# Performance work log

Hardware: AMD Instinct MI355X
Metric: run time of the kernel (lower is better)

Reference implementation:

```python
import jax, jax.numpy as jnp
import numpy as np

H = 1024   # hidden_size
B = 4096   # batch
C = 2      # num_classes

def setup_inputs() -> dict:
    key = jax.random.key(0)
    ks = jax.random.split(key, 12)
    s = 0.02
    return {
        "h": jax.random.normal(ks[0], (2, B, H), jnp.float32),
        "c": jax.random.normal(ks[1], (2, B, H), jnp.float32),
        # torch nn.LSTM params: W_ih_l0 (4H, C), W_hh_l0 (4H, H), biases (4H,)
        "W_ih0": jax.random.normal(ks[2], (4 * H, C), jnp.float32) * s,
        "W_hh0": jax.random.normal(ks[3], (4 * H, H), jnp.float32) * s,
        "b_ih0": jax.random.normal(ks[4], (4 * H,), jnp.float32) * s,
        "b_hh0": jax.random.normal(ks[5], (4 * H,), jnp.float32) * s,
        "W_ih1": jax.random.normal(ks[6], (4 * H, H), jnp.float32) * s,
        "W_hh1": jax.random.normal(ks[7], (4 * H, H), jnp.float32) * s,
        "b_ih1": jax.random.normal(ks[8], (4 * H,), jnp.float32) * s,
        "b_hh1": jax.random.normal(ks[9], (4 * H,), jnp.float32) * s,
        "fc_W": jax.random.normal(ks[10], (C, H), jnp.float32) * s,
        "fc_b": jax.random.normal(ks[11], (C,), jnp.float32) * s,
        "pred_len": 64,
    }

def _lstm_cell(gates, c_prev):
    # torch gate order: input, forget, cell(g), output
    i, f, g, o = jnp.split(gates, 4, axis=1)
    c_new = jax.nn.sigmoid(f) * c_prev + jax.nn.sigmoid(i) * jnp.tanh(g)
    h_new = jax.nn.sigmoid(o) * jnp.tanh(c_new)
    return h_new, c_new

def reference(h, c, W_ih0, W_hh0, b_ih0, b_hh0, W_ih1, W_hh1, b_ih1, b_hh1, fc_W, fc_b, pred_len):
    h0, h1 = h[0], h[1]
    c0, c1 = c[0], c[1]
    x0 = jnp.zeros((h0.shape[0], fc_W.shape[0]), h.dtype)  # (B, C)

    def step(carry, _):
        h0, c0, h1, c1, x = carry
        g0 = x @ W_ih0.T + b_ih0 + h0 @ W_hh0.T + b_hh0
        h0n, c0n = _lstm_cell(g0, c0)
        g1 = h0n @ W_ih1.T + b_ih1 + h1 @ W_hh1.T + b_hh1
        h1n, c1n = _lstm_cell(g1, c1)
        logit = h1n @ fc_W.T + fc_b                       # (B, C)
        # greedy argmax feedback (targets=None branch)
        x_next = jax.nn.one_hot(jnp.argmax(logit, axis=1), logit.shape[1], dtype=logit.dtype)
        return (h0n, c0n, h1n, c1n, x_next), logit

    _, logits = jax.lax.scan(step, (h0, c0, h1, c1, x0), None, length=pred_len)
    return jnp.transpose(logits, (1, 0, 2))  # (B, pred_len, C)
```

## Files before the change

### kernel.cpp

```cpp
#include <hip/hip_runtime.h>
#include <stdint.h>

#define H_ 1024
#define NG_ 4096

typedef float f32x4 __attribute__((ext_vector_type(4)));
typedef __bf16 bf16x8 __attribute__((ext_vector_type(8)));

__device__ __forceinline__ unsigned short f2bf(float f) {
  union { float f; uint32_t u; } v; v.f = f;
  uint32_t r = v.u + 0x7FFFu + ((v.u >> 16) & 1u);
  return (unsigned short)(r >> 16);
}
__device__ __forceinline__ float bf2f(unsigned short b) {
  union { uint32_t u; float f; } v; v.u = ((uint32_t)b) << 16; return v.f;
}

__device__ __forceinline__ void gload_lds16(const void* g, void* l) {
  __builtin_amdgcn_global_load_lds(
      (const __attribute__((address_space(1))) void*)g,
      (__attribute__((address_space(3))) void*)l, 16, 0, 0);
}

__device__ __forceinline__ float sigm(float x) { return 1.f / (1.f + __expf(-x)); }
__device__ __forceinline__ float tanh_(float x) { return 1.f - 2.f / (__expf(2.f * x) + 1.f); }

__global__ void prep_w0(const float* __restrict__ Whh0, unsigned short* __restrict__ Wr) {
  int i = (blockIdx.x * 256 + threadIdx.x) * 4;
  int r = i >> 10, k = i & 1023;
  int gate = (r >> 4) & 3;
  int j = ((r >> 6) << 4) + (r & 15);
  const float4 v = *(const float4*)(Whh0 + (size_t)(gate * H_ + j) * H_ + k);
  ushort4 o; o.x = f2bf(v.x); o.y = f2bf(v.y); o.z = f2bf(v.z); o.w = f2bf(v.w);
  *(ushort4*)(Wr + i) = o;
}

__global__ void prep_wcat(const float* __restrict__ Wih1, const float* __restrict__ Whh1,
                          unsigned short* __restrict__ Wr) {
  int i = (blockIdx.x * 256 + threadIdx.x) * 4;
  int r = i >> 11, k = i & 2047;
  int gate = (r >> 4) & 3;
  int j = ((r >> 6) << 4) + (r & 15);
  const float* src = (k < 1024) ? (Wih1 + (size_t)(gate * H_ + j) * H_ + k)
                                : (Whh1 + (size_t)(gate * H_ + j) * H_ + (k - 1024));
  const float4 v = *(const float4*)src;
  ushort4 o; o.x = f2bf(v.x); o.y = f2bf(v.y); o.z = f2bf(v.z); o.w = f2bf(v.w);
  *(ushort4*)(Wr + (size_t)r * 2048 + k) = o;
}

__global__ void prep_small(const float* __restrict__ Wih0,
                           const float* __restrict__ bih0, const float* __restrict__ bhh0,
                           const float* __restrict__ bih1, const float* __restrict__ bhh1,
                           float* __restrict__ bias0r, float* __restrict__ bias1r,
                           float* __restrict__ wi0r) {
  int r = blockIdx.x * 256 + threadIdx.x;
  int gate = (r >> 4) & 3;
  int j = ((r >> 6) << 4) + (r & 15);
  int old = gate * H_ + j;
  bias0r[r] = bih0[old] + bhh0[old];
  bias1r[r] = bih1[old] + bhh1[old];
  wi0r[r * 2 + 0] = Wih0[old * 2 + 0];
  wi0r[r * 2 + 1] = Wih0[old * 2 + 1];
}

__global__ void prep_state(const float* __restrict__ h, const float* __restrict__ c,
                           unsigned short* __restrict__ h0b, unsigned short* __restrict__ h1b,
                           float* __restrict__ c0, float* __restrict__ c1, int bh) {
  int i = (blockIdx.x * 256 + threadIdx.x) * 4;
  float4 a = *(const float4*)(h + i);
  float4 b = *(const float4*)(h + (size_t)bh + i);
  ushort4 oa; oa.x = f2bf(a.x); oa.y = f2bf(a.y); oa.z = f2bf(a.z); oa.w = f2bf(a.w);
  ushort4 ob; ob.x = f2bf(b.x); ob.y = f2bf(b.y); ob.z = f2bf(b.z); ob.w = f2bf(b.w);
  *(ushort4*)(h0b + i) = oa;
  *(ushort4*)(h1b + i) = ob;
  *(float4*)(c0 + i) = *(const float4*)(c + i);
  *(float4*)(c1 + i) = *(const float4*)(c + (size_t)bh + i);
}

__global__ void lstm_gemm_cell(const unsigned short* __restrict__ A0,
                               const unsigned short* __restrict__ A1,
                               int Ktot,
                               const unsigned short* __restrict__ Bw,
                               const float* __restrict__ biasr,
                               const float* __restrict__ wi0r,
                               const int* __restrict__ xidx,
                               int have_x,
                               float* __restrict__ Cst,
                               unsigned short* __restrict__ Hout) {
  __shared__ unsigned short As[128 * 64];
  __shared__ unsigned short Bs[128 * 64];
  const int tid  = threadIdx.x;
  const int lane = tid & 63;
  const int wv   = tid >> 6;
  const int wm   = wv >> 1, wn = wv & 1;
  const int tile_m = blockIdx.y * 128;
  const int tile_n = blockIdx.x * 128;

  f32x4 acc[4][4];
#pragma unroll
  for (int m = 0; m < 4; ++m)
#pragma unroll
    for (int n = 0; n < 4; ++n) acc[m][n] = (f32x4)0.f;

  const int lrow = lane >> 3;
  const int lk   = (lane & 7) * 8;

  const int nk = Ktot >> 6;
  for (int kt = 0; kt < nk; ++kt) {
    const int k0 = kt << 6;
    const unsigned short* Ap; int kl;
    if (k0 < 1024) { Ap = A0; kl = k0; } else { Ap = A1; kl = k0 - 1024; }
#pragma unroll
    for (int i = 0; i < 4; ++i) {
      int chunk = wv * 4 + i;
      int row = chunk * 8 + lrow;
      gload_lds16(Ap + (size_t)(tile_m + row) * H_ + kl + lk, (void*)&As[chunk * 512]);
    }
#pragma unroll
    for (int i = 0; i < 4; ++i) {
      int chunk = wv * 4 + i;
      int row = chunk * 8 + lrow;
      gload_lds16(Bw + (size_t)(tile_n + row) * Ktot + k0 + lk, (void*)&Bs[chunk * 512]);
    }
    __syncthreads();

    const char* Ab = (const char*)As;
    const char* Bb = (const char*)Bs;
    const int arow = wm * 64 + (lane & 15);
    const int brow = wn * 64 + (lane & 15);
    const int koff = (lane >> 4) * 16;
#pragma unroll
    for (int ks = 0; ks < 2; ++ks) {
      bf16x8 af[4], bfr[4];
#pragma unroll
      for (int m = 0; m < 4; ++m)
        af[m] = *(const bf16x8*)(Ab + (arow + m * 16) * 128 + ks * 64 + koff);
#pragma unroll
      for (int n = 0; n < 4; ++n)
        bfr[n] = *(const bf16x8*)(Bb + (brow + n * 16) * 128 + ks * 64 + koff);
#pragma unroll
      for (int m = 0; m < 4; ++m)
#pragma unroll
        for (int n = 0; n < 4; ++n)
          acc[m][n] = __builtin_amdgcn_mfma_f32_16x16x32_bf16(af[m], bfr[n], acc[m][n], 0, 0, 0);
    }
    __syncthreads();
  }

  const int cl = lane & 15;
  const int rq = (lane >> 4) * 4;
  const int jgrp = (tile_n >> 6) + wn;
  const int j = jgrp * 16 + cl;
  float bias[4], w0v[4] = {0,0,0,0}, w1v[4] = {0,0,0,0};
#pragma unroll
  for (int n = 0; n < 4; ++n) {
    int colr = tile_n + wn * 64 + n * 16 + cl;
    bias[n] = biasr[colr];
    if (have_x) { w0v[n] = wi0r[colr * 2]; w1v[n] = wi0r[colr * 2 + 1]; }
  }
#pragma unroll
  for (int m = 0; m < 4; ++m) {
#pragma unroll
    for (int q = 0; q < 4; ++q) {
      int row = tile_m + wm * 64 + m * 16 + rq + q;
      float gi = acc[m][0][q] + bias[0];
      float gf = acc[m][1][q] + bias[1];
      float gg = acc[m][2][q] + bias[2];
      float go = acc[m][3][q] + bias[3];
      if (have_x) {
        int x = xidx[row];
        gi += x ? w1v[0] : w0v[0];
        gf += x ? w1v[1] : w0v[1];
        gg += x ? w1v[2] : w0v[2];
        go += x ? w1v[3] : w0v[3];
      }
      size_t off = (size_t)row * H_ + j;
      float cp = Cst[off];
      float cn = sigm(gf) * cp + sigm(gi) * tanh_(gg);
      float hn = sigm(go) * tanh_(cn);
      Cst[off] = cn;
      Hout[off] = f2bf(hn);
    }
  }
}

__global__ void fc_argmax(const unsigned short* __restrict__ h1,
                          const float* __restrict__ fcW, const float* __restrict__ fcb,
                          float* __restrict__ out, int* __restrict__ xidx,
                          int t, int pred_len) {
  const int lane = threadIdx.x & 63;
  const int wv = threadIdx.x >> 6;
  const int row = blockIdx.x * 4 + wv;
  const unsigned short* hp = h1 + (size_t)row * H_ + lane * 16;
  float d0 = 0.f, d1 = 0.f;
#pragma unroll
  for (int u = 0; u < 2; ++u) {
    ushort4 ha = *(const ushort4*)(hp + u * 8);
    ushort4 hb = *(const ushort4*)(hp + u * 8 + 4);
    float hv[8] = { bf2f(ha.x), bf2f(ha.y), bf2f(ha.z), bf2f(ha.w),
                    bf2f(hb.x), bf2f(hb.y), bf2f(hb.z), bf2f(hb.w) };
#pragma unroll
    for (int e = 0; e < 8; ++e) {
      int k = lane * 16 + u * 8 + e;
      d0 += hv[e] * fcW[k];
      d1 += hv[e] * fcW[H_ + k];
    }
  }
#pragma unroll
  for (int off = 32; off > 0; off >>= 1) {
    d0 += __shfl_xor(d0, off);
    d1 += __shfl_xor(d1, off);
  }
  if (lane == 0) {
    d0 += fcb[0]; d1 += fcb[1];
    size_t o = ((size_t)row * pred_len + t) * 2;
    out[o] = d0; out[o + 1] = d1;
    xidx[row] = (d1 > d0) ? 1 : 0;
  }
}

extern "C" void kernel_launch(void* const* d_in, const int* in_sizes, int n_in,
                              void* d_out, int out_size, void* d_ws, size_t ws_size,
                              hipStream_t stream) {
  const float* h     = (const float*)d_in[0];
  const float* c     = (const float*)d_in[1];
  const float* Wih0  = (const float*)d_in[2];
  const float* Whh0  = (const float*)d_in[3];
  const float* bih0  = (const float*)d_in[4];
  const float* bhh0  = (const float*)d_in[5];
  const float* Wih1  = (const float*)d_in[6];
  const float* Whh1  = (const float*)d_in[7];
  const float* bih1  = (const float*)d_in[8];
  const float* bhh1  = (const float*)d_in[9];
  const float* fcW   = (const float*)d_in[10];
  const float* fcb   = (const float*)d_in[11];

  const int B = in_sizes[0] / (2 * H_);
  const int pred_len = out_size / (B * 2);
  const int BH = B * H_;

  size_t off = 0;
  auto carve = [&](size_t bytes) -> void* {
    void* p = (char*)d_ws + off;
    off += (bytes + 255) & ~(size_t)255;
    return p;
  };
  unsigned short* Whh0r = (unsigned short*)carve((size_t)NG_ * 1024 * 2);
  unsigned short* Wcatr = (unsigned short*)carve((size_t)NG_ * 2048 * 2);
  unsigned short* h0b[2], *h1b[2];
  h0b[0] = (unsigned short*)carve((size_t)BH * 2);
  h0b[1] = (unsigned short*)carve((size_t)BH * 2);
  h1b[0] = (unsigned short*)carve((size_t)BH * 2);
  h1b[1] = (unsigned short*)carve((size_t)BH * 2);
  float* c0 = (float*)carve((size_t)BH * 4);
  float* c1 = (float*)carve((size_t)BH * 4);
  float* bias0r = (float*)carve(NG_ * 4);
  float* bias1r = (float*)carve(NG_ * 4);
  float* wi0r   = (float*)carve(NG_ * 2 * 4);
  int*   xidx   = (int*)carve(B * 4);

  hipLaunchKernelGGL(prep_w0,   dim3((NG_ * 1024 / 4) / 256), dim3(256), 0, stream, Whh0, Whh0r);
  hipLaunchKernelGGL(prep_wcat, dim3((NG_ * 2048 / 4) / 256), dim3(256), 0, stream, Wih1, Whh1, Wcatr);
  hipLaunchKernelGGL(prep_small, dim3(NG_ / 256), dim3(256), 0, stream,
                     Wih0, bih0, bhh0, bih1, bhh1, bias0r, bias1r, wi0r);
  hipLaunchKernelGGL(prep_state, dim3((BH / 4) / 256), dim3(256), 0, stream,
                     h, c, h0b[0], h1b[0], c0, c1, BH);

  dim3 ggrid(NG_ / 128, B / 128);
  dim3 gblk(256);
  float* out = (float*)d_out;

  for (int t = 0; t < pred_len; ++t) {
    const int cur = t & 1, nxt = cur ^ 1;
    hipLaunchKernelGGL(lstm_gemm_cell, ggrid, gblk, 0, stream,
                       h0b[cur], (const unsigned short*)nullptr, 1024, Whh0r,
                       bias0r, wi0r, xidx, (t > 0) ? 1 : 0, c0, h0b[nxt]);
    hipLaunchKernelGGL(lstm_gemm_cell, ggrid, gblk, 0, stream,
                       h0b[nxt], h1b[cur], 2048, Wcatr,
                       bias1r, (const float*)nullptr, (const int*)nullptr, 0, c1, h1b[nxt]);
    hipLaunchKernelGGL(fc_argmax, dim3(B / 4), dim3(256), 0, stream,
                       h1b[nxt], fcW, fcb, out, xidx, t, pred_len);
  }
}
```

Measured before the change: 8.484 ms.

## Use 256x256 tiles with double-buffered swizzled LDS and async prefetch

The fused LSTM GEMM+cell kernel moves from 128x128 tiles with 4 waves to 256x256 tiles with 8 waves. Global-to-LDS loads are double-buffered two K-steps ahead using explicit waitcnt and barriers, and the LDS layout gets an XOR swizzle to avoid bank conflicts. The aim is to hide load latency behind MFMA and raise data reuse per byte. The cost is 128 KB of LDS and 256 grid blocks per launch, which lowers occupancy and may leave many CUs idle.

```diff
diff --git a/kernel.cpp b/kernel.cpp
--- a/kernel.cpp
+++ b/kernel.cpp
@@ -77,81 +77,116 @@
   *(float4*)(c1 + i) = *(const float4*)(c + (size_t)bh + i);
 }
 
-__global__ void lstm_gemm_cell(const unsigned short* __restrict__ A0,
-                               const unsigned short* __restrict__ A1,
-                               int Ktot,
-                               const unsigned short* __restrict__ Bw,
-                               const float* __restrict__ biasr,
-                               const float* __restrict__ wi0r,
-                               const int* __restrict__ xidx,
-                               int have_x,
-                               float* __restrict__ Cst,
-                               unsigned short* __restrict__ Hout) {
-  __shared__ unsigned short As[128 * 64];
-  __shared__ unsigned short Bs[128 * 64];
+__global__ void __launch_bounds__(512, 2)
+lstm_gemm_cell(const unsigned short* __restrict__ A0,
+               const unsigned short* __restrict__ A1,
+               int Ktot,
+               const unsigned short* __restrict__ Bw,
+               const float* __restrict__ biasr,
+               const float* __restrict__ wi0r,
+               const int* __restrict__ xidx,
+               int have_x,
+               float* __restrict__ Cst,
+               unsigned short* __restrict__ Hout) {
+  __shared__ unsigned short As[2][256 * 64];
+  __shared__ unsigned short Bs[2][256 * 64];
+
   const int tid  = threadIdx.x;
   const int lane = tid & 63;
   const int wv   = tid >> 6;
-  const int wm   = wv >> 1, wn = wv & 1;
-  const int tile_m = blockIdx.y * 128;
-  const int tile_n = blockIdx.x * 128;
-
-  f32x4 acc[4][4];
-#pragma unroll
-  for (int m = 0; m < 4; ++m)
+  const int wm   = wv >> 2;
+  const int wn   = wv & 3;
+  const int tile_m = blockIdx.y * 256;
+  const int tile_n = blockIdx.x * 256;
+
+  const int rowt = tid >> 3;
+  const int cb8  = (tid & 7) * 8;
+  const int ce   = (((tid & 7) ^ (rowt & 7)) * 8);
+
+  const int NK = Ktot >> 6;
+
+  auto stage = [&](int d, int kt) {
+    const int kb = kt << 6;
+    const unsigned short* Ap = A0; int kl = kb;
+    if (kb >= 1024) { Ap = A1; kl = kb - 1024; }
+#pragma unroll
+    for (int i = 0; i < 4; ++i) {
+      const int row = i * 64 + rowt;
+      gload_lds16(Ap + (size_t)(tile_m + row) * H_ + kl + ce, (void*)&As[d][row * 64 + cb8]);
+    }
+#pragma unroll
+    for (int i = 0; i < 4; ++i) {
+      const int row = i * 64 + rowt;
+      gload_lds16(Bw + (size_t)(tile_n + row) * (size_t)Ktot + kb + ce, (void*)&Bs[d][row * 64 + cb8]);
+    }
+  };
+
+  f32x4 acc[8][4];
+#pragma unroll
+  for (int m = 0; m < 8; ++m)
 #pragma unroll
     for (int n = 0; n < 4; ++n) acc[m][n] = (f32x4)0.f;
 
-  const int lrow = lane >> 3;
-  const int lk   = (lane & 7) * 8;
-
-  const int nk = Ktot >> 6;
-  for (int kt = 0; kt < nk; ++kt) {
-    const int k0 = kt << 6;
-    const unsigned short* Ap; int kl;
-    if (k0 < 1024) { Ap = A0; kl = k0; } else { Ap = A1; kl = k0 - 1024; }
-#pragma unroll
-    for (int i = 0; i < 4; ++i) {
-      int chunk = wv * 4 + i;
-      int row = chunk * 8 + lrow;
-      gload_lds16(Ap + (size_t)(tile_m + row) * H_ + kl + lk, (void*)&As[chunk * 512]);
-    }
-#pragma unroll
-    for (int i = 0; i < 4; ++i) {
-      int chunk = wv * 4 + i;
-      int row = chunk * 8 + lrow;
-      gload_lds16(Bw + (size_t)(tile_n + row) * Ktot + k0 + lk, (void*)&Bs[chunk * 512]);
-    }
-    __syncthreads();
-
-    const char* Ab = (const char*)As;
-    const char* Bb = (const char*)Bs;
-    const int arow = wm * 64 + (lane & 15);
-    const int brow = wn * 64 + (lane & 15);
-    const int koff = (lane >> 4) * 16;
-#pragma unroll
-    for (int ks = 0; ks < 2; ++ks) {
-      bf16x8 af[4], bfr[4];
-#pragma unroll
-      for (int m = 0; m < 4; ++m)
-        af[m] = *(const bf16x8*)(Ab + (arow + m * 16) * 128 + ks * 64 + koff);
+  const int cl  = lane & 15;
+  const int khi = lane >> 4;
+  const int Xn  = lane & 7;
+  const int ksw0 = ((0 + khi) ^ Xn) * 16;
+  const int ksw1 = ((4 + khi) ^ Xn) * 16;
+
+  stage(0, 0);
+  stage(1, 1);
+  asm volatile("s_waitcnt vmcnt(8)" ::: "memory");
+  __builtin_amdgcn_sched_barrier(0);
+  __builtin_amdgcn_s_barrier();
+
+  for (int kt = 0; kt < NK; ++kt) {
+    const int cur = kt & 1;
+    const char* Abase = (const char*)&As[cur][0] + (wm * 128 + cl) * 128;
+    const char* Bbase = (const char*)&Bs[cur][0] + (wn * 64 + cl) * 128;
+
+    bf16x8 af0[8], af1[8], bf0[4], bf1[4];
+#pragma unroll
+    for (int m = 0; m < 8; ++m) {
+      af0[m] = *(const bf16x8*)(Abase + m * 2048 + ksw0);
+      af1[m] = *(const bf16x8*)(Abase + m * 2048 + ksw1);
+    }
+#pragma unroll
+    for (int n = 0; n < 4; ++n) {
+      bf0[n] = *(const bf16x8*)(Bbase + n * 2048 + ksw0);
+      bf1[n] = *(const bf16x8*)(Bbase + n * 2048 + ksw1);
+    }
+
+    asm volatile("s_waitcnt lgkmcnt(0)" ::: "memory");
+    __builtin_amdgcn_sched_barrier(0);
+    __builtin_amdgcn_s_barrier();
+
+    if (kt + 2 < NK) {
+      stage(cur, kt + 2);
+      asm volatile("s_waitcnt vmcnt(8)" ::: "memory");
+    } else {
+      asm volatile("s_waitcnt vmcnt(0)" ::: "memory");
+    }
+    __builtin_amdgcn_sched_barrier(0);
+
+    __builtin_amdgcn_s_setprio(1);
+#pragma unroll
+    for (int m = 0; m < 8; ++m)
 #pragma unroll
       for (int n = 0; n < 4; ++n)
-        bfr[n] = *(const bf16x8*)(Bb + (brow + n * 16) * 128 + ks * 64 + koff);
-#pragma unroll
-      for (int m = 0; m < 4; ++m)
-#pragma unroll
-        for (int n = 0; n < 4; ++n)
-          acc[m][n] = __builtin_amdgcn_mfma_f32_16x16x32_bf16(af[m], bfr[n], acc[m][n], 0, 0, 0);
-    }
-    __syncthreads();
-  }
-
-  const int cl = lane & 15;
-  const int rq = (lane >> 4) * 4;
+        acc[m][n] = __builtin_amdgcn_mfma_f32_16x16x32_bf16(af0[m], bf0[n], acc[m][n], 0, 0, 0);
+#pragma unroll
+    for (int m = 0; m < 8; ++m)
+#pragma unroll
+      for (int n = 0; n < 4; ++n)
+        acc[m][n] = __builtin_amdgcn_mfma_f32_16x16x32_bf16(af1[m], bf1[n], acc[m][n], 0, 0, 0);
+    __builtin_amdgcn_s_setprio(0);
+
+    __builtin_amdgcn_s_barrier();
+  }
+
   const int jgrp = (tile_n >> 6) + wn;
   const int j = jgrp * 16 + cl;
-  float bias[4], w0v[4] = {0,0,0,0}, w1v[4] = {0,0,0,0};
+  float bias[4], w0v[4] = {0, 0, 0, 0}, w1v[4] = {0, 0, 0, 0};
 #pragma unroll
   for (int n = 0; n < 4; ++n) {
     int colr = tile_n + wn * 64 + n * 16 + cl;
@@ -159,10 +194,10 @@
     if (have_x) { w0v[n] = wi0r[colr * 2]; w1v[n] = wi0r[colr * 2 + 1]; }
   }
 #pragma unroll
-  for (int m = 0; m < 4; ++m) {
+  for (int m = 0; m < 8; ++m) {
 #pragma unroll
     for (int q = 0; q < 4; ++q) {
-      int row = tile_m + wm * 64 + m * 16 + rq + q;
+      int row = tile_m + wm * 128 + m * 16 + khi * 4 + q;
       float gi = acc[m][0][q] + bias[0];
       float gf = acc[m][1][q] + bias[1];
       float gg = acc[m][2][q] + bias[2];
@@ -266,8 +301,8 @@
   hipLaunchKernelGGL(prep_state, dim3((BH / 4) / 256), dim3(256), 0, stream,
                      h, c, h0b[0], h1b[0], c0, c1, BH);
 
-  dim3 ggrid(NG_ / 128, B / 128);
-  dim3 gblk(256);
+  dim3 ggrid(NG_ / 256, B / 256);
+  dim3 gblk(512);
   float* out = (float*)d_out;
 
   for (int t = 0; t < pred_len; ++t) {
```

Result: faster. 8.121 ms (-4.3%).

## Shrink GEMM tile to 64x128 with BK=32, swizzled LDS, and occupancy hint

Applied to the files above, without the earlier changes.

Reduces the per-block M tile from 128 to 64 and the K step from 64 to 32, halving accumulator registers and LDS use. Adds an XOR swizzle on the LDS write and read offsets to avoid bank conflicts, and sets launch bounds to target six blocks per CU. The grid doubles to 2048 blocks, which aims to improve occupancy and latency hiding across the many CUs. In exchange there is less data reuse per block, twice as many barriers per K, and more global traffic for the B operand.

```diff
diff --git a/kernel.cpp b/kernel.cpp
--- a/kernel.cpp
+++ b/kernel.cpp
@@ -77,81 +77,77 @@
   *(float4*)(c1 + i) = *(const float4*)(c + (size_t)bh + i);
 }
 
-__global__ void lstm_gemm_cell(const unsigned short* __restrict__ A0,
-                               const unsigned short* __restrict__ A1,
-                               int Ktot,
-                               const unsigned short* __restrict__ Bw,
-                               const float* __restrict__ biasr,
-                               const float* __restrict__ wi0r,
-                               const int* __restrict__ xidx,
-                               int have_x,
-                               float* __restrict__ Cst,
-                               unsigned short* __restrict__ Hout) {
-  __shared__ unsigned short As[128 * 64];
-  __shared__ unsigned short Bs[128 * 64];
+__global__ void __launch_bounds__(256, 6)
+lstm_gemm_cell(const unsigned short* __restrict__ A0,
+               const unsigned short* __restrict__ A1,
+               int Ktot,
+               const unsigned short* __restrict__ Bw,
+               const float* __restrict__ biasr,
+               const float* __restrict__ wi0r,
+               const int* __restrict__ xidx,
+               int have_x,
+               float* __restrict__ Cst,
+               unsigned short* __restrict__ Hout) {
+  __shared__ unsigned short As[64 * 32];
+  __shared__ unsigned short Bs[128 * 32];
   const int tid  = threadIdx.x;
   const int lane = tid & 63;
   const int wv   = tid >> 6;
   const int wm   = wv >> 1, wn = wv & 1;
-  const int tile_m = blockIdx.y * 128;
+  const int tile_m = blockIdx.y * 64;
   const int tile_n = blockIdx.x * 128;
 
-  f32x4 acc[4][4];
-#pragma unroll
-  for (int m = 0; m < 4; ++m)
+  f32x4 acc[2][4];
+#pragma unroll
+  for (int m = 0; m < 2; ++m)
 #pragma unroll
     for (int n = 0; n < 4; ++n) acc[m][n] = (f32x4)0.f;
 
-  const int lrow = lane >> 3;
-  const int lk   = (lane & 7) * 8;
-
-  const int nk = Ktot >> 6;
+  const int lrow16 = lane >> 2;
+  const int lk     = (((lane & 3) ^ ((lane >> 3) & 3)) * 8);
+
+  const int cl  = lane & 15;
+  const int khi = lane >> 4;
+  const int ksw = ((khi ^ ((lane >> 1) & 3)) * 16);
+
+  const int nk = Ktot >> 5;
   for (int kt = 0; kt < nk; ++kt) {
-    const int k0 = kt << 6;
+    const int k0 = kt << 5;
     const unsigned short* Ap; int kl;
     if (k0 < 1024) { Ap = A0; kl = k0; } else { Ap = A1; kl = k0 - 1024; }
-#pragma unroll
-    for (int i = 0; i < 4; ++i) {
-      int chunk = wv * 4 + i;
-      int row = chunk * 8 + lrow;
-      gload_lds16(Ap + (size_t)(tile_m + row) * H_ + kl + lk, (void*)&As[chunk * 512]);
-    }
-#pragma unroll
-    for (int i = 0; i < 4; ++i) {
-      int chunk = wv * 4 + i;
-      int row = chunk * 8 + lrow;
-      gload_lds16(Bw + (size_t)(tile_n + row) * Ktot + k0 + lk, (void*)&Bs[chunk * 512]);
+    {
+      const int row = wv * 16 + lrow16;
+      gload_lds16(Ap + (size_t)(tile_m + row) * H_ + kl + lk, (void*)&As[wv * 512]);
+    }
+#pragma unroll
+    for (int i = 0; i < 2; ++i) {
+      const int c2 = wv + i * 4;
+      const int row = c2 * 16 + lrow16;
+      gload_lds16(Bw + (size_t)(tile_n + row) * Ktot + k0 + lk, (void*)&Bs[c2 * 512]);
     }
     __syncthreads();
 
     const char* Ab = (const char*)As;
     const char* Bb = (const char*)Bs;
-    const int arow = wm * 64 + (lane & 15);
-    const int brow = wn * 64 + (lane & 15);
-    const int koff = (lane >> 4) * 16;
-#pragma unroll
-    for (int ks = 0; ks < 2; ++ks) {
-      bf16x8 af[4], bfr[4];
-#pragma unroll
-      for (int m = 0; m < 4; ++m)
-        af[m] = *(const bf16x8*)(Ab + (arow + m * 16) * 128 + ks * 64 + koff);
+    bf16x8 af[2], bfr[4];
+#pragma unroll
+    for (int m = 0; m < 2; ++m)
+      af[m] = *(const bf16x8*)(Ab + (wm * 32 + m * 16 + cl) * 64 + ksw);
+#pragma unroll
+    for (int n = 0; n < 4; ++n)
+      bfr[n] = *(const bf16x8*)(Bb + (wn * 64 + n * 16 + cl) * 64 + ksw);
+#pragma unroll
+    for (int m = 0; m < 2; ++m)
 #pragma unroll
       for (int n = 0; n < 4; ++n)
-        bfr[n] = *(const bf16x8*)(Bb + (brow + n * 16) * 128 + ks * 64 + koff);
-#pragma unroll
-      for (int m = 0; m < 4; ++m)
-#pragma unroll
-        for (int n = 0; n < 4; ++n)
-          acc[m][n] = __builtin_amdgcn_mfma_f32_16x16x32_bf16(af[m], bfr[n], acc[m][n], 0, 0, 0);
-    }
+        acc[m][n] = __builtin_amdgcn_mfma_f32_16x16x32_bf16(af[m], bfr[n], acc[m][n], 0, 0, 0);
     __syncthreads();
   }
 
-  const int cl = lane & 15;
-  const int rq = (lane >> 4) * 4;
+  const int rq = khi * 4;
   const int jgrp = (tile_n >> 6) + wn;
   const int j = jgrp * 16 + cl;
-  float bias[4], w0v[4] = {0,0,0,0}, w1v[4] = {0,0,0,0};
+  float bias[4], w0v[4] = {0, 0, 0, 0}, w1v[4] = {0, 0, 0, 0};
 #pragma unroll
   for (int n = 0; n < 4; ++n) {
     int colr = tile_n + wn * 64 + n * 16 + cl;
@@ -159,10 +155,10 @@
     if (have_x) { w0v[n] = wi0r[colr * 2]; w1v[n] = wi0r[colr * 2 + 1]; }
   }
 #pragma unroll
-  for (int m = 0; m < 4; ++m) {
+  for (int m = 0; m < 2; ++m) {
 #pragma unroll
     for (int q = 0; q < 4; ++q) {
-      int row = tile_m + wm * 64 + m * 16 + rq + q;
+      int row = tile_m + wm * 32 + m * 16 + rq + q;
       float gi = acc[m][0][q] + bias[0];
       float gf = acc[m][1][q] + bias[1];
       float gg = acc[m][2][q] + bias[2];
@@ -266,7 +262,7 @@
   hipLaunchKernelGGL(prep_state, dim3((BH / 4) / 256), dim3(256), 0, stream,
                      h, c, h0b[0], h1b[0], c0, c1, BH);
 
-  dim3 ggrid(NG_ / 128, B / 128);
+  dim3 ggrid(NG_ / 128, B / 64);
   dim3 gblk(256);
   float* out = (float*)d_out;
 
```

Result: slower. 11.33 ms (+33.5%).
